# Optimization experiments

Measured on AMD Instinct MI355X. Metric: run time of the kernel, lower is better.

Reference implementation:

```python
import jax, jax.numpy as jnp
import numpy as np

MAX_SHIFT = 15
EPS = 1e-8


def setup_inputs() -> dict:
    key = jax.random.key(0)
    k1, k2 = jax.random.split(key)
    B, T = 2048, 2048
    preds = jax.random.normal(k1, (B, T), dtype=jnp.float32)
    targets = jax.random.normal(k2, (B, T), dtype=jnp.float32)
    return {"preds": preds, "targets": targets}


def reference(preds, targets):
    # targets statistics (shared across shifts)
    tc = targets - jnp.mean(targets, axis=1, keepdims=True)          # [B, T]
    std_t = jnp.sqrt(jnp.sum(tc * tc, axis=1) + EPS)                 # [B]

    shifts = jnp.arange(-MAX_SHIFT, MAX_SHIFT + 1)                   # [S]

    def pearson_for_shift(s):
        ps = jnp.roll(preds, s, axis=1)                              # [B, T]
        pc = ps - jnp.mean(ps, axis=1, keepdims=True)
        std_p = jnp.sqrt(jnp.sum(pc * pc, axis=1) + EPS)             # [B]
        cov = jnp.sum(pc * tc, axis=1)                               # [B]
        return cov / (std_p * std_t)

    pearsons = jax.vmap(pearson_for_shift)(shifts)                   # [S, B]
    best = jnp.maximum(jnp.max(pearsons, axis=0), -1.0)              # [B], init -1
    return 1.0 - jnp.mean(best)
```

## Files before the change

kernel.cpp:

```cpp
#include <hip/hip_runtime.h>

#define TLEN 2048
#define BROWS 2048
#define NSHIFT 31
#define MAXSH 15
#define BLOCK 256
#define EPSF 1e-8f

__device__ __forceinline__ int padidx12(int k) { return 12 * (k >> 3) + (k & 7); }

template<int CTRL, int RMASK, bool BC>
__device__ __forceinline__ float dpp_mov(float v, float old) {
    return __int_as_float(__builtin_amdgcn_update_dpp(
        __float_as_int(old), __float_as_int(v), CTRL, RMASK, 0xF, BC));
}
__device__ __forceinline__ float wave_sum_dpp(float v) {
    v += dpp_mov<0x111, 0xF, true>(v, 0.f);
    v += dpp_mov<0x112, 0xF, true>(v, 0.f);
    v += dpp_mov<0x114, 0xF, true>(v, 0.f);
    v += dpp_mov<0x118, 0xF, true>(v, 0.f);
    v += dpp_mov<0x142, 0xA, true>(v, 0.f);
    v += dpp_mov<0x143, 0xC, true>(v, 0.f);
    return v;
}
__device__ __forceinline__ float wave_max_dpp(float v) {
    v = fmaxf(v, dpp_mov<0x111, 0xF, false>(v, v));
    v = fmaxf(v, dpp_mov<0x112, 0xF, false>(v, v));
    v = fmaxf(v, dpp_mov<0x114, 0xF, false>(v, v));
    v = fmaxf(v, dpp_mov<0x118, 0xF, false>(v, v));
    v = fmaxf(v, dpp_mov<0x142, 0xA, false>(v, v));
    v = fmaxf(v, dpp_mov<0x143, 0xC, false>(v, v));
    return v;
}

__global__ void __launch_bounds__(BLOCK, 4)
pearson_rows_kernel(const float* __restrict__ preds,
                    const float* __restrict__ targets,
                    float* __restrict__ row_best)
{
    __shared__ float smem[3392];
    float* wsum = smem + 3120;
    float* rbuf = smem + 3376;

    const int tid  = threadIdx.x;
    const int wave = tid >> 6;
    const int lane = tid & 63;
    const int row  = blockIdx.x;
    const float* p_row = preds   + (size_t)row * TLEN;
    const float* t_row = targets + (size_t)row * TLEN;

    float pc[8];
    {
        float4 a = ((const float4*)p_row)[2 * tid];
        float4 b = ((const float4*)p_row)[2 * tid + 1];
        pc[0] = a.x; pc[1] = a.y; pc[2] = a.z; pc[3] = a.w;
        pc[4] = b.x; pc[5] = b.y; pc[6] = b.z; pc[7] = b.w;
    }
    float sp = 0.f, spp = 0.f;
    #pragma unroll
    for (int i = 0; i < 8; ++i) { sp += pc[i]; spp = fmaf(pc[i], pc[i], spp); }

    float st = 0.f, stt = 0.f;
    #pragma unroll
    for (int r = 0; r < 2; ++r) {
        int f4 = tid + r * BLOCK;
        float4 tv = ((const float4*)t_row)[f4];
        st  += tv.x + tv.y + tv.z + tv.w;
        stt = fmaf(tv.x, tv.x, stt); stt = fmaf(tv.y, tv.y, stt);
        stt = fmaf(tv.z, tv.z, stt); stt = fmaf(tv.w, tv.w, stt);
        int k = f4 * 4 + MAXSH;
        smem[padidx12(k)]     = tv.x;
        smem[padidx12(k + 1)] = tv.y;
        smem[padidx12(k + 2)] = tv.z;
        smem[padidx12(k + 3)] = tv.w;
    }
    if (tid < MAXSH) {
        smem[padidx12(tid)] = t_row[TLEN - MAXSH + tid];
    } else if (tid >= 32 && tid < 32 + MAXSH) {
        int i = tid - 32;
        smem[padidx12(TLEN + MAXSH + i)] = t_row[i];
    }

    sp  = wave_sum_dpp(sp);
    spp = wave_sum_dpp(spp);
    st  = wave_sum_dpp(st);
    stt = wave_sum_dpp(stt);
    if (lane == 63) {
        *(float4*)(rbuf + wave * 4) = make_float4(sp, spp, st, stt);
    }
    __syncthreads();

    float w[38];
    {
        const float* g = smem + 12 * tid;
        #pragma unroll
        for (int q = 0; q < 4; ++q) {
            float4 a = *(const float4*)(g + 12 * q);
            float4 b = *(const float4*)(g + 12 * q + 4);
            w[8*q + 0] = a.x; w[8*q + 1] = a.y; w[8*q + 2] = a.z; w[8*q + 3] = a.w;
            w[8*q + 4] = b.x; w[8*q + 5] = b.y; w[8*q + 6] = b.z; w[8*q + 7] = b.w;
        }
        float4 c = *(const float4*)(g + 48);
        float2 e = *(const float2*)(g + 52);
        w[32] = c.x; w[33] = c.y; w[34] = c.z; w[35] = c.w;
        w[36] = e.x; w[37] = e.y;
        #pragma unroll
        for (int d = 0; d < 38; ++d) asm volatile("" : "+v"(w[d]));
    }

    float acc[NSHIFT];
    #pragma unroll
    for (int s = 0; s < NSHIFT; ++s) acc[s] = 0.f;
    #pragma unroll
    for (int m = 0; m < 8; ++m) {
        #pragma unroll
        for (int s = 0; s < NSHIFT; ++s) acc[s] = fmaf(pc[m], w[m + s], acc[s]);
    }

    #pragma unroll
    for (int s = 0; s < NSHIFT; ++s) acc[s] = wave_sum_dpp(acc[s]);
    if (lane == 63) {
        float* dst = wsum + wave * 64;
        *(float4*)(dst +  0) = make_float4(acc[0],  acc[1],  acc[2],  acc[3]);
        *(float4*)(dst +  4) = make_float4(acc[4],  acc[5],  acc[6],  acc[7]);
        *(float4*)(dst +  8) = make_float4(acc[8],  acc[9],  acc[10], acc[11]);
        *(float4*)(dst + 12) = make_float4(acc[12], acc[13], acc[14], acc[15]);
        *(float4*)(dst + 16) = make_float4(acc[16], acc[17], acc[18], acc[19]);
        *(float4*)(dst + 20) = make_float4(acc[20], acc[21], acc[22], acc[23]);
        *(float4*)(dst + 24) = make_float4(acc[24], acc[25], acc[26], acc[27]);
        *(float2*)(dst + 28) = make_float2(acc[28], acc[29]);
        dst[30] = acc[30];
    }
    __syncthreads();

    if (wave == 0) {
        float dot = wsum[lane] + wsum[64 + lane] + wsum[128 + lane] + wsum[192 + lane];
        float4 r0 = *(const float4*)(rbuf + 0);
        float4 r1 = *(const float4*)(rbuf + 4);
        float4 r2 = *(const float4*)(rbuf + 8);
        float4 r3 = *(const float4*)(rbuf + 12);
        float SP  = r0.x + r1.x + r2.x + r3.x;
        float SPP = r0.y + r1.y + r2.y + r3.y;
        float ST  = r0.z + r1.z + r2.z + r3.z;
        float STT = r0.w + r1.w + r2.w + r3.w;
        const float invT = 1.0f / TLEN;
        float mp = SP * invT, mt = ST * invT;
        float varp = SPP - (float)TLEN * mp * mp;
        float vart = STT - (float)TLEN * mt * mt;
        float corr = (float)TLEN * mp * mt;
        float pear = (dot - corr) * rsqrtf((varp + EPSF) * (vart + EPSF));
        float v = (lane < NSHIFT) ? pear : -3.0e38f;
        v = wave_max_dpp(v);
        if (lane == 63) row_best[row] = fmaxf(v, -1.0f);
    }
}

__global__ void __launch_bounds__(BLOCK)
pearson_finalize_kernel(const float* __restrict__ row_best, float* __restrict__ out)
{
    __shared__ float r[4];
    const int tid = threadIdx.x, wave = tid >> 6, lane = tid & 63;
    float4 a = ((const float4*)row_best)[tid];
    float4 b = ((const float4*)row_best)[tid + BLOCK];
    float s = (a.x + a.y) + (a.z + a.w) + (b.x + b.y) + (b.z + b.w);
    s = wave_sum_dpp(s);
    if (lane == 63) r[wave] = s;
    __syncthreads();
    if (tid == 0)
        out[0] = 1.0f - (r[0] + r[1] + r[2] + r[3]) * (1.0f / (float)BROWS);
}

extern "C" void kernel_launch(void* const* d_in, const int* in_sizes, int n_in,
                              void* d_out, int out_size, void* d_ws, size_t ws_size,
                              hipStream_t stream) {
    const float* preds   = (const float*)d_in[0];
    const float* targets = (const float*)d_in[1];
    float* row_best = (float*)d_ws;
    float* out      = (float*)d_out;
    pearson_rows_kernel<<<BROWS, BLOCK, 0, stream>>>(preds, targets, row_best);
    pearson_finalize_kernel<<<1, BLOCK, 0, stream>>>(row_best, out);
}
```

Before: 80.90 us.

## Fuse final reduction via atomicAdd and hoist all global loads early

```diff
diff --git a/kernel.cpp b/kernel.cpp
--- a/kernel.cpp
+++ b/kernel.cpp
@@ -34,9 +34,9 @@
 }
 
 __global__ void __launch_bounds__(BLOCK, 4)
-pearson_rows_kernel(const float* __restrict__ preds,
-                    const float* __restrict__ targets,
-                    float* __restrict__ row_best)
+pearson_fused_kernel(const float* __restrict__ preds,
+                     const float* __restrict__ targets,
+                     float* __restrict__ out)
 {
     __shared__ float smem[3392];
     float* wsum = smem + 3120;
@@ -49,37 +49,42 @@
     const float* p_row = preds   + (size_t)row * TLEN;
     const float* t_row = targets + (size_t)row * TLEN;
 
+    float4 tv0 = ((const float4*)t_row)[tid];
+    float4 tv1 = ((const float4*)t_row)[tid + BLOCK];
+    float hl = 0.f, hr = 0.f;
+    if (tid < MAXSH)                      hl = t_row[TLEN - MAXSH + tid];
+    else if (tid >= 32 && tid < 32 + MAXSH) hr = t_row[tid - 32];
+    float4 pa = ((const float4*)p_row)[2 * tid];
+    float4 pb = ((const float4*)p_row)[2 * tid + 1];
+
+    {
+        int k = tid * 4 + MAXSH;
+        smem[padidx12(k)]     = tv0.x;
+        smem[padidx12(k + 1)] = tv0.y;
+        smem[padidx12(k + 2)] = tv0.z;
+        smem[padidx12(k + 3)] = tv0.w;
+        k = (tid + BLOCK) * 4 + MAXSH;
+        smem[padidx12(k)]     = tv1.x;
+        smem[padidx12(k + 1)] = tv1.y;
+        smem[padidx12(k + 2)] = tv1.z;
+        smem[padidx12(k + 3)] = tv1.w;
+        if (tid < MAXSH)                        smem[padidx12(tid)] = hl;
+        else if (tid >= 32 && tid < 32 + MAXSH) smem[padidx12(TLEN + MAXSH + tid - 32)] = hr;
+    }
+    float st = 0.f, stt = 0.f;
+    st += tv0.x + tv0.y + tv0.z + tv0.w;
+    st += tv1.x + tv1.y + tv1.z + tv1.w;
+    stt = fmaf(tv0.x, tv0.x, stt); stt = fmaf(tv0.y, tv0.y, stt);
+    stt = fmaf(tv0.z, tv0.z, stt); stt = fmaf(tv0.w, tv0.w, stt);
+    stt = fmaf(tv1.x, tv1.x, stt); stt = fmaf(tv1.y, tv1.y, stt);
+    stt = fmaf(tv1.z, tv1.z, stt); stt = fmaf(tv1.w, tv1.w, stt);
+
     float pc[8];
-    {
-        float4 a = ((const float4*)p_row)[2 * tid];
-        float4 b = ((const float4*)p_row)[2 * tid + 1];
-        pc[0] = a.x; pc[1] = a.y; pc[2] = a.z; pc[3] = a.w;
-        pc[4] = b.x; pc[5] = b.y; pc[6] = b.z; pc[7] = b.w;
-    }
+    pc[0] = pa.x; pc[1] = pa.y; pc[2] = pa.z; pc[3] = pa.w;
+    pc[4] = pb.x; pc[5] = pb.y; pc[6] = pb.z; pc[7] = pb.w;
     float sp = 0.f, spp = 0.f;
     #pragma unroll
     for (int i = 0; i < 8; ++i) { sp += pc[i]; spp = fmaf(pc[i], pc[i], spp); }
-
-    float st = 0.f, stt = 0.f;
-    #pragma unroll
-    for (int r = 0; r < 2; ++r) {
-        int f4 = tid + r * BLOCK;
-        float4 tv = ((const float4*)t_row)[f4];
-        st  += tv.x + tv.y + tv.z + tv.w;
-        stt = fmaf(tv.x, tv.x, stt); stt = fmaf(tv.y, tv.y, stt);
-        stt = fmaf(tv.z, tv.z, stt); stt = fmaf(tv.w, tv.w, stt);
-        int k = f4 * 4 + MAXSH;
-        smem[padidx12(k)]     = tv.x;
-        smem[padidx12(k + 1)] = tv.y;
-        smem[padidx12(k + 2)] = tv.z;
-        smem[padidx12(k + 3)] = tv.w;
-    }
-    if (tid < MAXSH) {
-        smem[padidx12(tid)] = t_row[TLEN - MAXSH + tid];
-    } else if (tid >= 32 && tid < 32 + MAXSH) {
-        int i = tid - 32;
-        smem[padidx12(TLEN + MAXSH + i)] = t_row[i];
-    }
 
     sp  = wave_sum_dpp(sp);
     spp = wave_sum_dpp(spp);
@@ -151,23 +156,11 @@
         float pear = (dot - corr) * rsqrtf((varp + EPSF) * (vart + EPSF));
         float v = (lane < NSHIFT) ? pear : -3.0e38f;
         v = wave_max_dpp(v);
-        if (lane == 63) row_best[row] = fmaxf(v, -1.0f);
+        if (lane == 63) {
+            float best = fmaxf(v, -1.0f);
+            atomicAdd(out, (1.0f - best) * (1.0f / (float)BROWS));
+        }
     }
-}
-
-__global__ void __launch_bounds__(BLOCK)
-pearson_finalize_kernel(const float* __restrict__ row_best, float* __restrict__ out)
-{
-    __shared__ float r[4];
-    const int tid = threadIdx.x, wave = tid >> 6, lane = tid & 63;
-    float4 a = ((const float4*)row_best)[tid];
-    float4 b = ((const float4*)row_best)[tid + BLOCK];
-    float s = (a.x + a.y) + (a.z + a.w) + (b.x + b.y) + (b.z + b.w);
-    s = wave_sum_dpp(s);
-    if (lane == 63) r[wave] = s;
-    __syncthreads();
-    if (tid == 0)
-        out[0] = 1.0f - (r[0] + r[1] + r[2] + r[3]) * (1.0f / (float)BROWS);
 }
 
 extern "C" void kernel_launch(void* const* d_in, const int* in_sizes, int n_in,
@@ -175,8 +168,7 @@
                               hipStream_t stream) {
     const float* preds   = (const float*)d_in[0];
     const float* targets = (const float*)d_in[1];
-    float* row_best = (float*)d_ws;
-    float* out      = (float*)d_out;
-    pearson_rows_kernel<<<BROWS, BLOCK, 0, stream>>>(preds, targets, row_best);
-    pearson_finalize_kernel<<<1, BLOCK, 0, stream>>>(row_best, out);
+    float* out = (float*)d_out;
+    hipMemsetAsync(out, 0, sizeof(float), stream);
+    pearson_fused_kernel<<<BROWS, BLOCK, 0, stream>>>(preds, targets, out);
 }
```

Measured after the change: 98.31 us. 21.5% more time.

## Assign one row per wavefront and drop block-level barriers

Applied to the files above, without the earlier changes.

```diff
diff --git a/kernel.cpp b/kernel.cpp
--- a/kernel.cpp
+++ b/kernel.cpp
@@ -5,6 +5,10 @@
 #define NSHIFT 31
 #define MAXSH 15
 #define BLOCK 256
+#define ROWSPB 4
+#define NCHUNK 4
+#define GROUPS_PER_ROW 260
+#define ROW_LDS (12 * GROUPS_PER_ROW)
 #define EPSF 1e-8f
 
 __device__ __forceinline__ int padidx12(int k) { return 12 * (k >> 3) + (k & 7); }
@@ -23,76 +27,73 @@
     v += dpp_mov<0x143, 0xC, true>(v, 0.f);
     return v;
 }
-__device__ __forceinline__ float wave_max_dpp(float v) {
-    v = fmaxf(v, dpp_mov<0x111, 0xF, false>(v, v));
-    v = fmaxf(v, dpp_mov<0x112, 0xF, false>(v, v));
-    v = fmaxf(v, dpp_mov<0x114, 0xF, false>(v, v));
-    v = fmaxf(v, dpp_mov<0x118, 0xF, false>(v, v));
-    v = fmaxf(v, dpp_mov<0x142, 0xA, false>(v, v));
-    v = fmaxf(v, dpp_mov<0x143, 0xC, false>(v, v));
-    return v;
-}
 
-__global__ void __launch_bounds__(BLOCK, 4)
+__global__ void __launch_bounds__(BLOCK, 2)
 pearson_rows_kernel(const float* __restrict__ preds,
                     const float* __restrict__ targets,
                     float* __restrict__ row_best)
 {
-    __shared__ float smem[3392];
-    float* wsum = smem + 3120;
-    float* rbuf = smem + 3376;
+    __shared__ float smem[ROWSPB * ROW_LDS];
 
     const int tid  = threadIdx.x;
     const int wave = tid >> 6;
     const int lane = tid & 63;
-    const int row  = blockIdx.x;
+    const int row  = blockIdx.x * ROWSPB + wave;
+    float* S = smem + wave * ROW_LDS;
     const float* p_row = preds   + (size_t)row * TLEN;
     const float* t_row = targets + (size_t)row * TLEN;
 
-    float pc[8];
-    {
-        float4 a = ((const float4*)p_row)[2 * tid];
-        float4 b = ((const float4*)p_row)[2 * tid + 1];
-        pc[0] = a.x; pc[1] = a.y; pc[2] = a.z; pc[3] = a.w;
-        pc[4] = b.x; pc[5] = b.y; pc[6] = b.z; pc[7] = b.w;
+    float4 tv[8];
+    #pragma unroll
+    for (int r = 0; r < 8; ++r) tv[r] = ((const float4*)t_row)[lane + 64 * r];
+    float hl = 0.f, hr = 0.f;
+    if (lane < MAXSH)                hl = t_row[TLEN - MAXSH + lane];
+    else if (lane >= 16 && lane < 31) hr = t_row[lane - 16];
+    float4 pv[2 * NCHUNK];
+    #pragma unroll
+    for (int c = 0; c < NCHUNK; ++c) {
+        pv[2*c]     = ((const float4*)p_row)[2 * lane + 128 * c];
+        pv[2*c + 1] = ((const float4*)p_row)[2 * lane + 128 * c + 1];
+    }
+
+    #pragma unroll
+    for (int r = 0; r < 8; ++r) {
+        int k = 4 * (lane + 64 * r) + MAXSH;
+        S[padidx12(k)]     = tv[r].x;
+        S[padidx12(k + 1)] = tv[r].y;
+        S[padidx12(k + 2)] = tv[r].z;
+        S[padidx12(k + 3)] = tv[r].w;
+    }
+    if (lane < MAXSH)                S[padidx12(lane)] = hl;
+    else if (lane >= 16 && lane < 31) S[padidx12(TLEN + MAXSH + lane - 16)] = hr;
+    asm volatile("s_waitcnt lgkmcnt(0)" ::: "memory");
+
+    float st = 0.f, stt = 0.f;
+    #pragma unroll
+    for (int r = 0; r < 8; ++r) {
+        st += tv[r].x + tv[r].y + tv[r].z + tv[r].w;
+        stt = fmaf(tv[r].x, tv[r].x, stt); stt = fmaf(tv[r].y, tv[r].y, stt);
+        stt = fmaf(tv[r].z, tv[r].z, stt); stt = fmaf(tv[r].w, tv[r].w, stt);
     }
     float sp = 0.f, spp = 0.f;
     #pragma unroll
-    for (int i = 0; i < 8; ++i) { sp += pc[i]; spp = fmaf(pc[i], pc[i], spp); }
-
-    float st = 0.f, stt = 0.f;
-    #pragma unroll
-    for (int r = 0; r < 2; ++r) {
-        int f4 = tid + r * BLOCK;
-        float4 tv = ((const float4*)t_row)[f4];
-        st  += tv.x + tv.y + tv.z + tv.w;
-        stt = fmaf(tv.x, tv.x, stt); stt = fmaf(tv.y, tv.y, stt);
-        stt = fmaf(tv.z, tv.z, stt); stt = fmaf(tv.w, tv.w, stt);
-        int k = f4 * 4 + MAXSH;
-        smem[padidx12(k)]     = tv.x;
-        smem[padidx12(k + 1)] = tv.y;
-        smem[padidx12(k + 2)] = tv.z;
-        smem[padidx12(k + 3)] = tv.w;
+    for (int i = 0; i < 2 * NCHUNK; ++i) {
+        sp += pv[i].x + pv[i].y + pv[i].z + pv[i].w;
+        spp = fmaf(pv[i].x, pv[i].x, spp); spp = fmaf(pv[i].y, pv[i].y, spp);
+        spp = fmaf(pv[i].z, pv[i].z, spp); spp = fmaf(pv[i].w, pv[i].w, spp);
     }
-    if (tid < MAXSH) {
-        smem[padidx12(tid)] = t_row[TLEN - MAXSH + tid];
-    } else if (tid >= 32 && tid < 32 + MAXSH) {
-        int i = tid - 32;
-        smem[padidx12(TLEN + MAXSH + i)] = t_row[i];
-    }
-
     sp  = wave_sum_dpp(sp);
     spp = wave_sum_dpp(spp);
     st  = wave_sum_dpp(st);
     stt = wave_sum_dpp(stt);
-    if (lane == 63) {
-        *(float4*)(rbuf + wave * 4) = make_float4(sp, spp, st, stt);
-    }
-    __syncthreads();
 
-    float w[38];
-    {
-        const float* g = smem + 12 * tid;
+    float acc[NSHIFT];
+    #pragma unroll
+    for (int s = 0; s < NSHIFT; ++s) acc[s] = 0.f;
+    #pragma unroll 1
+    for (int c = 0; c < NCHUNK; ++c) {
+        float w[38];
+        const float* g = S + 12 * (lane + 64 * c);
         #pragma unroll
         for (int q = 0; q < 4; ++q) {
             float4 a = *(const float4*)(g + 12 * q);
@@ -100,58 +101,38 @@
             w[8*q + 0] = a.x; w[8*q + 1] = a.y; w[8*q + 2] = a.z; w[8*q + 3] = a.w;
             w[8*q + 4] = b.x; w[8*q + 5] = b.y; w[8*q + 6] = b.z; w[8*q + 7] = b.w;
         }
-        float4 c = *(const float4*)(g + 48);
-        float2 e = *(const float2*)(g + 52);
-        w[32] = c.x; w[33] = c.y; w[34] = c.z; w[35] = c.w;
-        w[36] = e.x; w[37] = e.y;
+        float4 cc = *(const float4*)(g + 48);
+        float2 ee = *(const float2*)(g + 52);
+        w[32] = cc.x; w[33] = cc.y; w[34] = cc.z; w[35] = cc.w;
+        w[36] = ee.x; w[37] = ee.y;
         #pragma unroll
         for (int d = 0; d < 38; ++d) asm volatile("" : "+v"(w[d]));
-    }
 
-    float acc[NSHIFT];
-    #pragma unroll
-    for (int s = 0; s < NSHIFT; ++s) acc[s] = 0.f;
-    #pragma unroll
-    for (int m = 0; m < 8; ++m) {
+        float pcc[8];
+        pcc[0] = pv[2*c].x;   pcc[1] = pv[2*c].y;
+        pcc[2] = pv[2*c].z;   pcc[3] = pv[2*c].w;
+        pcc[4] = pv[2*c+1].x; pcc[5] = pv[2*c+1].y;
+        pcc[6] = pv[2*c+1].z; pcc[7] = pv[2*c+1].w;
         #pragma unroll
-        for (int s = 0; s < NSHIFT; ++s) acc[s] = fmaf(pc[m], w[m + s], acc[s]);
+        for (int m = 0; m < 8; ++m) {
+            #pragma unroll
+            for (int s = 0; s < NSHIFT; ++s) acc[s] = fmaf(pcc[m], w[m + s], acc[s]);
+        }
     }
 
     #pragma unroll
     for (int s = 0; s < NSHIFT; ++s) acc[s] = wave_sum_dpp(acc[s]);
     if (lane == 63) {
-        float* dst = wsum + wave * 64;
-        *(float4*)(dst +  0) = make_float4(acc[0],  acc[1],  acc[2],  acc[3]);
-        *(float4*)(dst +  4) = make_float4(acc[4],  acc[5],  acc[6],  acc[7]);
-        *(float4*)(dst +  8) = make_float4(acc[8],  acc[9],  acc[10], acc[11]);
-        *(float4*)(dst + 12) = make_float4(acc[12], acc[13], acc[14], acc[15]);
-        *(float4*)(dst + 16) = make_float4(acc[16], acc[17], acc[18], acc[19]);
-        *(float4*)(dst + 20) = make_float4(acc[20], acc[21], acc[22], acc[23]);
-        *(float4*)(dst + 24) = make_float4(acc[24], acc[25], acc[26], acc[27]);
-        *(float2*)(dst + 28) = make_float2(acc[28], acc[29]);
-        dst[30] = acc[30];
-    }
-    __syncthreads();
-
-    if (wave == 0) {
-        float dot = wsum[lane] + wsum[64 + lane] + wsum[128 + lane] + wsum[192 + lane];
-        float4 r0 = *(const float4*)(rbuf + 0);
-        float4 r1 = *(const float4*)(rbuf + 4);
-        float4 r2 = *(const float4*)(rbuf + 8);
-        float4 r3 = *(const float4*)(rbuf + 12);
-        float SP  = r0.x + r1.x + r2.x + r3.x;
-        float SPP = r0.y + r1.y + r2.y + r3.y;
-        float ST  = r0.z + r1.z + r2.z + r3.z;
-        float STT = r0.w + r1.w + r2.w + r3.w;
+        float dmax = acc[0];
+        #pragma unroll
+        for (int s = 1; s < NSHIFT; ++s) dmax = fmaxf(dmax, acc[s]);
         const float invT = 1.0f / TLEN;
-        float mp = SP * invT, mt = ST * invT;
-        float varp = SPP - (float)TLEN * mp * mp;
-        float vart = STT - (float)TLEN * mt * mt;
+        float mp = sp * invT, mt = st * invT;
+        float varp = spp - (float)TLEN * mp * mp;
+        float vart = stt - (float)TLEN * mt * mt;
         float corr = (float)TLEN * mp * mt;
-        float pear = (dot - corr) * rsqrtf((varp + EPSF) * (vart + EPSF));
-        float v = (lane < NSHIFT) ? pear : -3.0e38f;
-        v = wave_max_dpp(v);
-        if (lane == 63) row_best[row] = fmaxf(v, -1.0f);
+        float pear = (dmax - corr) * rsqrtf((varp + EPSF) * (vart + EPSF));
+        row_best[row] = fmaxf(pear, -1.0f);
     }
 }
 
@@ -177,6 +158,6 @@
     const float* targets = (const float*)d_in[1];
     float* row_best = (float*)d_ws;
     float* out      = (float*)d_out;
-    pearson_rows_kernel<<<BROWS, BLOCK, 0, stream>>>(preds, targets, row_best);
+    pearson_rows_kernel<<<BROWS / ROWSPB, BLOCK, 0, stream>>>(preds, targets, row_best);
     pearson_finalize_kernel<<<1, BLOCK, 0, stream>>>(row_best, out);
 }
```

After: 86.82 us. 1.07x slower.

## Process four rows per block with register prefetch of the next row

Applied to the files above, without the earlier changes.

```diff
diff --git a/kernel.cpp b/kernel.cpp
--- a/kernel.cpp
+++ b/kernel.cpp
@@ -3,8 +3,8 @@
 #define TLEN 2048
 #define BROWS 2048
 #define NSHIFT 31
-#define MAXSH 15
 #define BLOCK 256
+#define ROWSPB 4
 #define EPSF 1e-8f
 
 __device__ __forceinline__ int padidx12(int k) { return 12 * (k >> 3) + (k & 7); }
@@ -33,125 +33,139 @@
     return v;
 }
 
-__global__ void __launch_bounds__(BLOCK, 4)
+__global__ void __launch_bounds__(BLOCK, 2)
 pearson_rows_kernel(const float* __restrict__ preds,
                     const float* __restrict__ targets,
                     float* __restrict__ row_best)
 {
-    __shared__ float smem[3392];
-    float* wsum = smem + 3120;
-    float* rbuf = smem + 3376;
+    __shared__ float smem[3408];
+    float* wsum  = smem + 3120;
+    float* rbufs = smem + 3376;
 
     const int tid  = threadIdx.x;
     const int wave = tid >> 6;
     const int lane = tid & 63;
-    const int row  = blockIdx.x;
-    const float* p_row = preds   + (size_t)row * TLEN;
-    const float* t_row = targets + (size_t)row * TLEN;
+    const int row0 = blockIdx.x * ROWSPB;
 
-    float pc[8];
+    const bool haloL = (tid < 4);
+    const bool haloR = (tid >= 32 && tid < 36);
     {
-        float4 a = ((const float4*)p_row)[2 * tid];
-        float4 b = ((const float4*)p_row)[2 * tid + 1];
-        pc[0] = a.x; pc[1] = a.y; pc[2] = a.z; pc[3] = a.w;
-        pc[4] = b.x; pc[5] = b.y; pc[6] = b.z; pc[7] = b.w;
     }
-    float sp = 0.f, spp = 0.f;
-    #pragma unroll
-    for (int i = 0; i < 8; ++i) { sp += pc[i]; spp = fmaf(pc[i], pc[i], spp); }
+    const float* t0 = targets + (size_t)row0 * TLEN;
+    const float* p0 = preds   + (size_t)row0 * TLEN;
+    float4 tv0 = ((const float4*)t0)[tid];
+    float4 tv1 = ((const float4*)t0)[tid + BLOCK];
+    float4 hv  = make_float4(0.f, 0.f, 0.f, 0.f);
+    if (haloL)      hv = *(const float4*)(t0 + 2032 + 4 * tid);
+    else if (haloR) hv = *(const float4*)(t0 + 4 * (tid - 32));
+    float4 pa = ((const float4*)p0)[2 * tid];
+    float4 pb = ((const float4*)p0)[2 * tid + 1];
 
-    float st = 0.f, stt = 0.f;
-    #pragma unroll
-    for (int r = 0; r < 2; ++r) {
-        int f4 = tid + r * BLOCK;
-        float4 tv = ((const float4*)t_row)[f4];
-        st  += tv.x + tv.y + tv.z + tv.w;
-        stt = fmaf(tv.x, tv.x, stt); stt = fmaf(tv.y, tv.y, stt);
-        stt = fmaf(tv.z, tv.z, stt); stt = fmaf(tv.w, tv.w, stt);
-        int k = f4 * 4 + MAXSH;
-        smem[padidx12(k)]     = tv.x;
-        smem[padidx12(k + 1)] = tv.y;
-        smem[padidx12(k + 2)] = tv.z;
-        smem[padidx12(k + 3)] = tv.w;
-    }
-    if (tid < MAXSH) {
-        smem[padidx12(tid)] = t_row[TLEN - MAXSH + tid];
-    } else if (tid >= 32 && tid < 32 + MAXSH) {
-        int i = tid - 32;
-        smem[padidx12(TLEN + MAXSH + i)] = t_row[i];
-    }
+    #pragma unroll 1
+    for (int it = 0; it < ROWSPB; ++it) {
+        const int row = row0 + it;
+        float* rbuf = rbufs + (it & 1) * 16;
 
-    sp  = wave_sum_dpp(sp);
-    spp = wave_sum_dpp(spp);
-    st  = wave_sum_dpp(st);
-    stt = wave_sum_dpp(stt);
-    if (lane == 63) {
-        *(float4*)(rbuf + wave * 4) = make_float4(sp, spp, st, stt);
-    }
-    __syncthreads();
+        *(float4*)(smem + padidx12(4 * tid + 16))   = tv0;
+        *(float4*)(smem + padidx12(4 * tid + 1040)) = tv1;
+        if (haloL)      *(float4*)(smem + padidx12(4 * tid)) = hv;
+        else if (haloR) *(float4*)(smem + padidx12(2064 + 4 * (tid - 32))) = hv;
 
-    float w[38];
-    {
-        const float* g = smem + 12 * tid;
+        float4 ntv0 = tv0, ntv1 = tv1, nhv = hv, npa = pa, npb = pb;
+        if (it + 1 < ROWSPB) {
+            const float* nt = targets + (size_t)(row + 1) * TLEN;
+            const float* np = preds   + (size_t)(row + 1) * TLEN;
+            ntv0 = ((const float4*)nt)[tid];
+            ntv1 = ((const float4*)nt)[tid + BLOCK];
+            if (haloL)      nhv = *(const float4*)(nt + 2032 + 4 * tid);
+            else if (haloR) nhv = *(const float4*)(nt + 4 * (tid - 32));
+            npa = ((const float4*)np)[2 * tid];
+            npb = ((const float4*)np)[2 * tid + 1];
+        }
+
+        float st  = (tv0.x + tv0.y) + (tv0.z + tv0.w) + (tv1.x + tv1.y) + (tv1.z + tv1.w);
+        float stt = 0.f, sp = 0.f, spp = 0.f;
+        stt = fmaf(tv0.x, tv0.x, stt); stt = fmaf(tv0.y, tv0.y, stt);
+        stt = fmaf(tv0.z, tv0.z, stt); stt = fmaf(tv0.w, tv0.w, stt);
+        stt = fmaf(tv1.x, tv1.x, stt); stt = fmaf(tv1.y, tv1.y, stt);
+        stt = fmaf(tv1.z, tv1.z, stt); stt = fmaf(tv1.w, tv1.w, stt);
+        sp  = (pa.x + pa.y) + (pa.z + pa.w) + (pb.x + pb.y) + (pb.z + pb.w);
+        spp = fmaf(pa.x, pa.x, spp); spp = fmaf(pa.y, pa.y, spp);
+        spp = fmaf(pa.z, pa.z, spp); spp = fmaf(pa.w, pa.w, spp);
+        spp = fmaf(pb.x, pb.x, spp); spp = fmaf(pb.y, pb.y, spp);
+        spp = fmaf(pb.z, pb.z, spp); spp = fmaf(pb.w, pb.w, spp);
+        sp  = wave_sum_dpp(sp);
+        spp = wave_sum_dpp(spp);
+        st  = wave_sum_dpp(st);
+        stt = wave_sum_dpp(stt);
+        if (lane == 63) *(float4*)(rbuf + wave * 4) = make_float4(sp, spp, st, stt);
+        __syncthreads();
+
+        float w[40];
+        {
+            const float* g = smem + 12 * tid;
+            #pragma unroll
+            for (int q = 0; q < 5; ++q) {
+                float4 a = *(const float4*)(g + 12 * q);
+                float4 b = *(const float4*)(g + 12 * q + 4);
+                w[8*q + 0] = a.x; w[8*q + 1] = a.y; w[8*q + 2] = a.z; w[8*q + 3] = a.w;
+                w[8*q + 4] = b.x; w[8*q + 5] = b.y; w[8*q + 6] = b.z; w[8*q + 7] = b.w;
+            }
+            #pragma unroll
+            for (int d = 1; d < 39; ++d) asm volatile("" : "+v"(w[d]));
+        }
+
+        float pc[8];
+        pc[0] = pa.x; pc[1] = pa.y; pc[2] = pa.z; pc[3] = pa.w;
+        pc[4] = pb.x; pc[5] = pb.y; pc[6] = pb.z; pc[7] = pb.w;
+        float acc[NSHIFT];
         #pragma unroll
-        for (int q = 0; q < 4; ++q) {
-            float4 a = *(const float4*)(g + 12 * q);
-            float4 b = *(const float4*)(g + 12 * q + 4);
-            w[8*q + 0] = a.x; w[8*q + 1] = a.y; w[8*q + 2] = a.z; w[8*q + 3] = a.w;
-            w[8*q + 4] = b.x; w[8*q + 5] = b.y; w[8*q + 6] = b.z; w[8*q + 7] = b.w;
+        for (int s = 0; s < NSHIFT; ++s) acc[s] = 0.f;
+        #pragma unroll
+        for (int m = 0; m < 8; ++m) {
+            #pragma unroll
+            for (int u = 0; u < NSHIFT; ++u)
+                acc[u] = fmaf(pc[m], w[m + u + 1], acc[u]);
         }
-        float4 c = *(const float4*)(g + 48);
-        float2 e = *(const float2*)(g + 52);
-        w[32] = c.x; w[33] = c.y; w[34] = c.z; w[35] = c.w;
-        w[36] = e.x; w[37] = e.y;
+
         #pragma unroll
-        for (int d = 0; d < 38; ++d) asm volatile("" : "+v"(w[d]));
-    }
+        for (int s = 0; s < NSHIFT; ++s) acc[s] = wave_sum_dpp(acc[s]);
+        if (lane == 63) {
+            float* dst = wsum + wave * 64;
+            *(float4*)(dst +  0) = make_float4(acc[0],  acc[1],  acc[2],  acc[3]);
+            *(float4*)(dst +  4) = make_float4(acc[4],  acc[5],  acc[6],  acc[7]);
+            *(float4*)(dst +  8) = make_float4(acc[8],  acc[9],  acc[10], acc[11]);
+            *(float4*)(dst + 12) = make_float4(acc[12], acc[13], acc[14], acc[15]);
+            *(float4*)(dst + 16) = make_float4(acc[16], acc[17], acc[18], acc[19]);
+            *(float4*)(dst + 20) = make_float4(acc[20], acc[21], acc[22], acc[23]);
+            *(float4*)(dst + 24) = make_float4(acc[24], acc[25], acc[26], acc[27]);
+            *(float2*)(dst + 28) = make_float2(acc[28], acc[29]);
+            dst[30] = acc[30];
+        }
+        __syncthreads();
 
-    float acc[NSHIFT];
-    #pragma unroll
-    for (int s = 0; s < NSHIFT; ++s) acc[s] = 0.f;
-    #pragma unroll
-    for (int m = 0; m < 8; ++m) {
-        #pragma unroll
-        for (int s = 0; s < NSHIFT; ++s) acc[s] = fmaf(pc[m], w[m + s], acc[s]);
-    }
+        if (wave == 0) {
+            float dot = wsum[lane] + wsum[64 + lane] + wsum[128 + lane] + wsum[192 + lane];
+            float4 r0 = *(const float4*)(rbuf + 0);
+            float4 r1 = *(const float4*)(rbuf + 4);
+            float4 r2 = *(const float4*)(rbuf + 8);
+            float4 r3 = *(const float4*)(rbuf + 12);
+            float SP  = r0.x + r1.x + r2.x + r3.x;
+            float SPP = r0.y + r1.y + r2.y + r3.y;
+            float ST  = r0.z + r1.z + r2.z + r3.z;
+            float STT = r0.w + r1.w + r2.w + r3.w;
+            const float invT = 1.0f / TLEN;
+            float mp = SP * invT, mt = ST * invT;
+            float varp = SPP - (float)TLEN * mp * mp;
+            float vart = STT - (float)TLEN * mt * mt;
+            float corr = (float)TLEN * mp * mt;
+            float pear = (dot - corr) * rsqrtf((varp + EPSF) * (vart + EPSF));
+            float v = (lane < NSHIFT) ? pear : -3.0e38f;
+            v = wave_max_dpp(v);
+            if (lane == 63) row_best[row] = fmaxf(v, -1.0f);
+        }
 
-    #pragma unroll
-    for (int s = 0; s < NSHIFT; ++s) acc[s] = wave_sum_dpp(acc[s]);
-    if (lane == 63) {
-        float* dst = wsum + wave * 64;
-        *(float4*)(dst +  0) = make_float4(acc[0],  acc[1],  acc[2],  acc[3]);
-        *(float4*)(dst +  4) = make_float4(acc[4],  acc[5],  acc[6],  acc[7]);
-        *(float4*)(dst +  8) = make_float4(acc[8],  acc[9],  acc[10], acc[11]);
-        *(float4*)(dst + 12) = make_float4(acc[12], acc[13], acc[14], acc[15]);
-        *(float4*)(dst + 16) = make_float4(acc[16], acc[17], acc[18], acc[19]);
-        *(float4*)(dst + 20) = make_float4(acc[20], acc[21], acc[22], acc[23]);
-        *(float4*)(dst + 24) = make_float4(acc[24], acc[25], acc[26], acc[27]);
-        *(float2*)(dst + 28) = make_float2(acc[28], acc[29]);
-        dst[30] = acc[30];
-    }
-    __syncthreads();
-
-    if (wave == 0) {
-        float dot = wsum[lane] + wsum[64 + lane] + wsum[128 + lane] + wsum[192 + lane];
-        float4 r0 = *(const float4*)(rbuf + 0);
-        float4 r1 = *(const float4*)(rbuf + 4);
-        float4 r2 = *(const float4*)(rbuf + 8);
-        float4 r3 = *(const float4*)(rbuf + 12);
-        float SP  = r0.x + r1.x + r2.x + r3.x;
-        float SPP = r0.y + r1.y + r2.y + r3.y;
-        float ST  = r0.z + r1.z + r2.z + r3.z;
-        float STT = r0.w + r1.w + r2.w + r3.w;
-        const float invT = 1.0f / TLEN;
-        float mp = SP * invT, mt = ST * invT;
-        float varp = SPP - (float)TLEN * mp * mp;
-        float vart = STT - (float)TLEN * mt * mt;
-        float corr = (float)TLEN * mp * mt;
-        float pear = (dot - corr) * rsqrtf((varp + EPSF) * (vart + EPSF));
-        float v = (lane < NSHIFT) ? pear : -3.0e38f;
-        v = wave_max_dpp(v);
-        if (lane == 63) row_best[row] = fmaxf(v, -1.0f);
+        tv0 = ntv0; tv1 = ntv1; hv = nhv; pa = npa; pb = npb;
     }
 }
 
@@ -177,6 +191,6 @@
     const float* targets = (const float*)d_in[1];
     float* row_best = (float*)d_ws;
     float* out      = (float*)d_out;
-    pearson_rows_kernel<<<BROWS, BLOCK, 0, stream>>>(preds, targets, row_best);
+    pearson_rows_kernel<<<BROWS / ROWSPB, BLOCK, 0, stream>>>(preds, targets, row_best);
     pearson_finalize_kernel<<<1, BLOCK, 0, stream>>>(row_best, out);
 }
```

Result: slower. 86.12 us (+6.5%).
